# Kernel tuning notes

Hardware: AMD Instinct MI355X
Metric: run time of the kernel (lower is better)

## Reference

```python
import jax, jax.numpy as jnp
import numpy as np

Q_MAX = 127.0  # int8 symmetric range for activations


def setup_inputs() -> dict:
    key = jax.random.key(0)
    k1, k2, k3, k4 = jax.random.split(key, 4)
    B, S, D_IN, D_OUT = 4, 2048, 4096, 4096
    x = jax.random.normal(k1, (B, S, D_IN), dtype=jnp.float32)
    # int8 weights stored as int32 in range [-127, 127]
    w_q = jax.random.randint(k2, (D_OUT, D_IN), -127, 128, dtype=jnp.int32)
    # per-output-channel weight dequant scale (small positive)
    w_scale = jax.random.uniform(k3, (D_OUT,), dtype=jnp.float32, minval=0.001, maxval=0.02)
    b = jax.random.normal(k4, (D_OUT,), dtype=jnp.float32)
    return {"x": x, "w_q": w_q, "w_scale": w_scale, "b": b}


def reference(x, w_q, w_scale, b):
    # dynamic per-token symmetric quantization of activations
    act_scale = jnp.maximum(jnp.max(jnp.abs(x), axis=-1, keepdims=True), 1e-8) / Q_MAX  # [B,S,1]
    x_q = jnp.clip(jnp.round(x / act_scale), -128.0, 127.0)  # int8-valued float
    acc = jnp.einsum("bsk,nk->bsn", x_q, w_q.astype(jnp.float32))  # [B,S,D_OUT]
    # dequantize: per-token act scale * per-channel weight scale, then bias
    y = acc * act_scale * w_scale + b
    return y
```

## Files before the change

### kernel.cpp

```cpp
#include <hip/hip_runtime.h>
#include <hip/hip_bf16.h>
#include <stdint.h>

typedef int v4i __attribute__((ext_vector_type(4)));

#define TOK 8192
#define DIN 4096
#define DOUT 4096

#define NT 32

__global__ __launch_bounds__(256) void quant_rows(const float* __restrict__ x,
                                                  int8_t* __restrict__ xq,
                                                  float* __restrict__ ascale) {
    const int row = blockIdx.x;
    const int t = threadIdx.x;
    const float* __restrict__ xr = x + (size_t)row * DIN;
    float4 v[4];
    float amax = 0.0f;
#pragma unroll
    for (int i = 0; i < 4; ++i) {
        v[i] = reinterpret_cast<const float4*>(xr)[t + 256 * i];
        amax = fmaxf(amax, fmaxf(fmaxf(fabsf(v[i].x), fabsf(v[i].y)),
                                 fmaxf(fabsf(v[i].z), fabsf(v[i].w))));
    }
#pragma unroll
    for (int off = 1; off < 64; off <<= 1)
        amax = fmaxf(amax, __shfl_xor(amax, off, 64));
    __shared__ float wmax[4];
    if ((t & 63) == 0) wmax[t >> 6] = amax;
    __syncthreads();
    amax = fmaxf(fmaxf(wmax[0], wmax[1]), fmaxf(wmax[2], wmax[3]));
    const float scale = fmaxf(amax, 1e-8f) / 127.0f;
    if (t == 0) ascale[row] = scale;
    uint32_t* __restrict__ qr = reinterpret_cast<uint32_t*>(xq + (size_t)row * DIN);
#pragma unroll
    for (int i = 0; i < 4; ++i) {
        int q0 = (int)fminf(fmaxf(rintf(v[i].x / scale), -128.0f), 127.0f);
        int q1 = (int)fminf(fmaxf(rintf(v[i].y / scale), -128.0f), 127.0f);
        int q2 = (int)fminf(fmaxf(rintf(v[i].z / scale), -128.0f), 127.0f);
        int q3 = (int)fminf(fmaxf(rintf(v[i].w / scale), -128.0f), 127.0f);
        qr[t + 256 * i] = (uint32_t)((q0 & 0xFF) | ((q1 & 0xFF) << 8) |
                                     ((q2 & 0xFF) << 16) | ((q3 & 0xFF) << 24));
    }
}

__global__ __launch_bounds__(256) void pack_w(const int* __restrict__ wq,
                                              uint32_t* __restrict__ w8) {
    const size_t i = (size_t)blockIdx.x * 256 + threadIdx.x;
    int4 a = reinterpret_cast<const int4*>(wq)[i];
    w8[i] = (uint32_t)((a.x & 0xFF) | ((a.y & 0xFF) << 8) |
                       ((a.z & 0xFF) << 16) | ((a.w & 0xFF) << 24));
}

__global__ __launch_bounds__(256, 2) void gemm_i8(const int8_t* __restrict__ A,
                                                  const int8_t* __restrict__ B,
                                                  const float* __restrict__ ascale,
                                                  const float* __restrict__ wscale,
                                                  const float* __restrict__ bias,
                                                  float* __restrict__ C) {
    __shared__ __attribute__((aligned(16))) uint8_t lds[65536];
    const int tid = threadIdx.x;
    const int bn = blockIdx.x, bm = blockIdx.y;

    const int srow = tid >> 3;
    const int sp = tid & 7;
    const size_t soff0 = (size_t)srow * DIN + (size_t)(((sp ^ (srow & 7)) * 16));
    const size_t soff1 = soff0 + (size_t)32 * DIN;
    const uint32_t dst0 = (uint32_t)tid * 16u;
    const uint32_t dst1 = dst0 + 4096u;
    const int8_t* gA = A + (size_t)bm * 128 * DIN;
    const int8_t* gB = B + (size_t)bn * 128 * DIN;

#define STAGE_HALF(gmat, rbase, bufv, h, ktc)                                            \
    do {                                                                                 \
        const int8_t* _s = (gmat) + ((size_t)(h)*64 * DIN) + ((size_t)(ktc)*128);        \
        const uint32_t _d = (rbase) + (uint32_t)(bufv)*16384u + (uint32_t)(h)*8192u;     \
        __builtin_amdgcn_global_load_lds(                                                \
            (const __attribute__((address_space(1))) void*)(_s + soff0),                 \
            (__attribute__((address_space(3))) void*)(&lds[_d + dst0]), 16, 0, 0);       \
        __builtin_amdgcn_global_load_lds(                                                \
            (const __attribute__((address_space(1))) void*)(_s + soff1),                 \
            (__attribute__((address_space(3))) void*)(&lds[_d + dst1]), 16, 0, 0);       \
    } while (0)

    const int wid = tid >> 6, l = tid & 63;
    const int wm = (wid >> 1) * 64;
    const int wn = (wid & 1) * 64;
    const int lr = l & 15, lg = l >> 4;
    const uint32_t koff0 = (uint32_t)(((lg) ^ (l & 7)) * 16);
    const uint32_t koff1 = (uint32_t)(((4 + lg) ^ (l & 7)) * 16);
    const uint32_t aRd = (uint32_t)((wm + lr) * 128);
    const uint32_t bRd = 32768u + (uint32_t)((wn + lr) * 128);
    const uint32_t a0_0 = aRd + koff0, a1_0 = aRd + koff1;
    const uint32_t a0_1 = a0_0 + 16384u, a1_1 = a1_0 + 16384u;
    const uint32_t b0_0 = bRd + koff0, b1_0 = bRd + koff1;
    const uint32_t b0_1 = b0_0 + 16384u, b1_1 = b1_0 + 16384u;

    v4i acc[4][4];
#pragma unroll
    for (int i = 0; i < 4; ++i)
#pragma unroll
        for (int j = 0; j < 4; ++j) acc[i][j] = (v4i){0, 0, 0, 0};

    v4i aT[2][2], aB[2][2], bL[2][2], bR[2][2];

#define DSR(d, b, o) asm volatile("ds_read_b128 %0, %1 offset:" o : "=v"(d) : "v"(b))

#define RD_AT(A0, A1)                                          \
    do {                                                       \
        DSR(aT[0][0], A0, "0");     DSR(aT[0][1], A1, "0");    \
        DSR(aT[1][0], A0, "2048");  DSR(aT[1][1], A1, "2048"); \
    } while (0)
#define RD_AB(A0, A1)                                          \
    do {                                                       \
        DSR(aB[0][0], A0, "4096");  DSR(aB[0][1], A1, "4096"); \
        DSR(aB[1][0], A0, "6144");  DSR(aB[1][1], A1, "6144"); \
    } while (0)
#define RD_BL(B0, B1)                                          \
    do {                                                       \
        DSR(bL[0][0], B0, "0");    DSR(bL[0][1], B1, "0");     \
        DSR(bL[1][0], B0, "2048"); DSR(bL[1][1], B1, "2048");  \
    } while (0)
#define RD_BR(B0, B1)                                          \
    do {                                                       \
        DSR(bR[0][0], B0, "4096"); DSR(bR[0][1], B1, "4096");  \
        DSR(bR[1][0], B0, "6144"); DSR(bR[1][1], B1, "6144");  \
    } while (0)

#define BAR() asm volatile("s_barrier" ::: "memory")
#define LGKM0()                                                \
    do {                                                       \
        asm volatile("s_waitcnt lgkmcnt(0)" ::: "memory");     \
        __builtin_amdgcn_sched_barrier(0);                     \
    } while (0)
#define PRIO1() __builtin_amdgcn_s_setprio(1)
#define PRIO0()                                \
    do {                                       \
        __builtin_amdgcn_sched_barrier(0);     \
        __builtin_amdgcn_s_setprio(0);         \
    } while (0)
#define VM(n) asm volatile("s_waitcnt vmcnt(" #n ")" ::: "memory")

#define MFMA_K(AF, BF, MB, NB)                                                           \
    do {                                                                                 \
        _Pragma("unroll") for (int kk = 0; kk < 2; ++kk)                                 \
        _Pragma("unroll") for (int mi = 0; mi < 2; ++mi)                                 \
        _Pragma("unroll") for (int ni = 0; ni < 2; ++ni) {                               \
            acc[(MB) + mi][(NB) + ni] = __builtin_amdgcn_mfma_i32_16x16x64_i8(           \
                AF[mi][kk], BF[ni][kk], acc[(MB) + mi][(NB) + ni], 0, 0, 0);             \
        }                                                                                \
    } while (0)

    STAGE_HALF(gA, 0u, 0, 0, 0);
    STAGE_HALF(gA, 0u, 0, 1, 0);
    STAGE_HALF(gB, 32768u, 0, 0, 0);
    STAGE_HALF(gB, 32768u, 0, 1, 0);
    STAGE_HALF(gA, 0u, 1, 0, 1);
    STAGE_HALF(gA, 0u, 1, 1, 1);
    VM(4);

    for (int t = 0; t < NT / 2; ++t) {
        const int cv = 2 * t + 1;
        const int cu2 = (2 * t + 2 < NT) ? 2 * t + 2 : NT - 1;
        const int cv2 = (2 * t + 3 < NT) ? 2 * t + 3 : NT - 1;

        BAR();
        STAGE_HALF(gB, 32768u, 1, 0, cv);
        RD_AT(a0_0, a1_0); RD_BL(b0_0, b1_0);
        LGKM0();
        PRIO1();
        RD_AB(a0_0, a1_0); RD_BR(b0_0, b1_0);
        MFMA_K(aT, bL, 0, 0);
        PRIO0();

        BAR();
        STAGE_HALF(gB, 32768u, 1, 1, cv);
        LGKM0();
        PRIO1(); MFMA_K(aT, bR, 0, 2); PRIO0();

        BAR();
        STAGE_HALF(gA, 0u, 0, 0, cu2);
        LGKM0();
        PRIO1(); MFMA_K(aB, bL, 2, 0); PRIO0();

        BAR();
        STAGE_HALF(gA, 0u, 0, 1, cu2);
        LGKM0();
        PRIO1(); MFMA_K(aB, bR, 2, 2); PRIO0();
        VM(4);

        BAR();
        STAGE_HALF(gB, 32768u, 0, 0, cu2);
        RD_AT(a0_1, a1_1); RD_BL(b0_1, b1_1);
        LGKM0();
        PRIO1();
        RD_AB(a0_1, a1_1); RD_BR(b0_1, b1_1);
        MFMA_K(aT, bL, 0, 0);
        PRIO0();

        BAR();
        STAGE_HALF(gB, 32768u, 0, 1, cu2);
        LGKM0();
        PRIO1(); MFMA_K(aT, bR, 0, 2); PRIO0();

        BAR();
        STAGE_HALF(gA, 0u, 1, 0, cv2);
        LGKM0();
        PRIO1(); MFMA_K(aB, bL, 2, 0); PRIO0();

        BAR();
        STAGE_HALF(gA, 0u, 1, 1, cv2);
        LGKM0();
        PRIO1(); MFMA_K(aB, bR, 2, 2); PRIO0();
        VM(4);
    }

    asm volatile("s_waitcnt lgkmcnt(0)" ::: "memory");
    VM(0);

    const int col0 = bn * 128 + wn + lr;
    float wsv[4], bbv[4];
#pragma unroll
    for (int ni = 0; ni < 4; ++ni) {
        wsv[ni] = wscale[col0 + ni * 16];
        bbv[ni] = bias[col0 + ni * 16];
    }
    const int rbase = bm * 128 + wm + lg * 4;
#pragma unroll
    for (int mi = 0; mi < 4; ++mi) {
#pragma unroll
        for (int r = 0; r < 4; ++r) {
            const int row = rbase + mi * 16 + r;
            const float as = ascale[row];
            float* __restrict__ crow = C + (size_t)row * DOUT;
#pragma unroll
            for (int ni = 0; ni < 4; ++ni) {
                crow[col0 + ni * 16] = (float)acc[mi][ni][r] * as * wsv[ni] + bbv[ni];
            }
        }
    }
#undef STAGE_HALF
#undef DSR
#undef RD_AT
#undef RD_AB
#undef RD_BL
#undef RD_BR
#undef BAR
#undef LGKM0
#undef PRIO1
#undef PRIO0
#undef VM
#undef MFMA_K
}

extern "C" void kernel_launch(void* const* d_in, const int* in_sizes, int n_in,
                              void* d_out, int out_size, void* d_ws, size_t ws_size,
                              hipStream_t stream) {
    const float* x = (const float*)d_in[0];
    const int* wq = (const int*)d_in[1];
    const float* wscale = (const float*)d_in[2];
    const float* bias = (const float*)d_in[3];
    float* out = (float*)d_out;

    int8_t* xq = (int8_t*)d_ws;
    int8_t* w8 = xq + (size_t)TOK * DIN;
    float* ascale = (float*)(w8 + (size_t)DOUT * DIN);

    quant_rows<<<TOK, 256, 0, stream>>>(x, xq, ascale);
    pack_w<<<(int)(((size_t)DOUT * DIN / 4) / 256), 256, 0, stream>>>(wq, (uint32_t*)w8);
    gemm_i8<<<dim3(DOUT / 128, TOK / 128), 256, 0, stream>>>(xq, w8, ascale, wscale, bias, out);
}
```

Baseline: 191.4 us.

## Halve GEMM K-tile to 64 to cut LDS and double occupancy

Shrinks the K tile of the int8 GEMM from 128 to 64 bytes. This halves LDS use to 32 KB and the fragment registers, so launch bounds can request 4 blocks per CU instead of 2. The staging swizzle, read offsets, wait counts and MFMA grouping are reworked to match. The main loop runs twice as many iterations with twice the barriers per unit of work, in exchange for more resident waves to hide latency.

```diff
diff --git a/kernel.cpp b/kernel.cpp
--- a/kernel.cpp
+++ b/kernel.cpp
@@ -8,7 +8,7 @@
 #define DIN 4096
 #define DOUT 4096
 
-#define NT 32
+#define NT 64
 
 __global__ __launch_bounds__(256) void quant_rows(const float* __restrict__ x,
                                                   int8_t* __restrict__ xq,
@@ -53,49 +53,41 @@
                        ((a.z & 0xFF) << 16) | ((a.w & 0xFF) << 24));
 }
 
-__global__ __launch_bounds__(256, 2) void gemm_i8(const int8_t* __restrict__ A,
+__global__ __launch_bounds__(256, 4) void gemm_i8(const int8_t* __restrict__ A,
                                                   const int8_t* __restrict__ B,
                                                   const float* __restrict__ ascale,
                                                   const float* __restrict__ wscale,
                                                   const float* __restrict__ bias,
                                                   float* __restrict__ C) {
-    __shared__ __attribute__((aligned(16))) uint8_t lds[65536];
+    __shared__ __attribute__((aligned(16))) uint8_t lds[32768];
     const int tid = threadIdx.x;
     const int bn = blockIdx.x, bm = blockIdx.y;
 
-    const int srow = tid >> 3;
-    const int sp = tid & 7;
-    const size_t soff0 = (size_t)srow * DIN + (size_t)(((sp ^ (srow & 7)) * 16));
-    const size_t soff1 = soff0 + (size_t)32 * DIN;
+    const int srow = tid >> 2;
+    const int sp = tid & 3;
+    const size_t soff0 = (size_t)srow * DIN + (size_t)(((sp ^ ((srow >> 1) & 3)) * 16));
     const uint32_t dst0 = (uint32_t)tid * 16u;
-    const uint32_t dst1 = dst0 + 4096u;
     const int8_t* gA = A + (size_t)bm * 128 * DIN;
     const int8_t* gB = B + (size_t)bn * 128 * DIN;
 
 #define STAGE_HALF(gmat, rbase, bufv, h, ktc)                                            \
     do {                                                                                 \
-        const int8_t* _s = (gmat) + ((size_t)(h)*64 * DIN) + ((size_t)(ktc)*128);        \
-        const uint32_t _d = (rbase) + (uint32_t)(bufv)*16384u + (uint32_t)(h)*8192u;     \
+        const int8_t* _s = (gmat) + ((size_t)(h)*64 * DIN) + ((size_t)(ktc)*64);         \
+        const uint32_t _d = (rbase) + (uint32_t)(bufv)*8192u + (uint32_t)(h)*4096u;      \
         __builtin_amdgcn_global_load_lds(                                                \
             (const __attribute__((address_space(1))) void*)(_s + soff0),                 \
             (__attribute__((address_space(3))) void*)(&lds[_d + dst0]), 16, 0, 0);       \
-        __builtin_amdgcn_global_load_lds(                                                \
-            (const __attribute__((address_space(1))) void*)(_s + soff1),                 \
-            (__attribute__((address_space(3))) void*)(&lds[_d + dst1]), 16, 0, 0);       \
     } while (0)
 
     const int wid = tid >> 6, l = tid & 63;
     const int wm = (wid >> 1) * 64;
     const int wn = (wid & 1) * 64;
     const int lr = l & 15, lg = l >> 4;
-    const uint32_t koff0 = (uint32_t)(((lg) ^ (l & 7)) * 16);
-    const uint32_t koff1 = (uint32_t)(((4 + lg) ^ (l & 7)) * 16);
-    const uint32_t aRd = (uint32_t)((wm + lr) * 128);
-    const uint32_t bRd = 32768u + (uint32_t)((wn + lr) * 128);
-    const uint32_t a0_0 = aRd + koff0, a1_0 = aRd + koff1;
-    const uint32_t a0_1 = a0_0 + 16384u, a1_1 = a1_0 + 16384u;
-    const uint32_t b0_0 = bRd + koff0, b1_0 = bRd + koff1;
-    const uint32_t b0_1 = b0_0 + 16384u, b1_1 = b1_0 + 16384u;
+    const uint32_t koff = (uint32_t)((lg ^ ((lr >> 1) & 3)) * 16);
+    const uint32_t aRd0 = (uint32_t)((wm + lr) * 64) + koff;
+    const uint32_t aRd1 = aRd0 + 8192u;
+    const uint32_t bRd0 = 16384u + (uint32_t)((wn + lr) * 64) + koff;
+    const uint32_t bRd1 = bRd0 + 8192u;
 
     v4i acc[4][4];
 #pragma unroll
@@ -103,30 +95,14 @@
 #pragma unroll
         for (int j = 0; j < 4; ++j) acc[i][j] = (v4i){0, 0, 0, 0};
 
-    v4i aT[2][2], aB[2][2], bL[2][2], bR[2][2];
+    v4i aT[2], aB[2], bL[2], bR[2];
 
 #define DSR(d, b, o) asm volatile("ds_read_b128 %0, %1 offset:" o : "=v"(d) : "v"(b))
 
-#define RD_AT(A0, A1)                                          \
-    do {                                                       \
-        DSR(aT[0][0], A0, "0");     DSR(aT[0][1], A1, "0");    \
-        DSR(aT[1][0], A0, "2048");  DSR(aT[1][1], A1, "2048"); \
-    } while (0)
-#define RD_AB(A0, A1)                                          \
-    do {                                                       \
-        DSR(aB[0][0], A0, "4096");  DSR(aB[0][1], A1, "4096"); \
-        DSR(aB[1][0], A0, "6144");  DSR(aB[1][1], A1, "6144"); \
-    } while (0)
-#define RD_BL(B0, B1)                                          \
-    do {                                                       \
-        DSR(bL[0][0], B0, "0");    DSR(bL[0][1], B1, "0");     \
-        DSR(bL[1][0], B0, "2048"); DSR(bL[1][1], B1, "2048");  \
-    } while (0)
-#define RD_BR(B0, B1)                                          \
-    do {                                                       \
-        DSR(bR[0][0], B0, "4096"); DSR(bR[0][1], B1, "4096");  \
-        DSR(bR[1][0], B0, "6144"); DSR(bR[1][1], B1, "6144");  \
-    } while (0)
+#define RD_AT(Ab) do { DSR(aT[0], Ab, "0");    DSR(aT[1], Ab, "1024"); } while (0)
+#define RD_AB(Ab) do { DSR(aB[0], Ab, "2048"); DSR(aB[1], Ab, "3072"); } while (0)
+#define RD_BL(Bb) do { DSR(bL[0], Bb, "0");    DSR(bL[1], Bb, "1024"); } while (0)
+#define RD_BR(Bb) do { DSR(bR[0], Bb, "2048"); DSR(bR[1], Bb, "3072"); } while (0)
 
 #define BAR() asm volatile("s_barrier" ::: "memory")
 #define LGKM0()                                                \
@@ -142,23 +118,22 @@
     } while (0)
 #define VM(n) asm volatile("s_waitcnt vmcnt(" #n ")" ::: "memory")
 
-#define MFMA_K(AF, BF, MB, NB)                                                           \
+#define MFMA_Q(AF, BF, MB, NB)                                                           \
     do {                                                                                 \
-        _Pragma("unroll") for (int kk = 0; kk < 2; ++kk)                                 \
         _Pragma("unroll") for (int mi = 0; mi < 2; ++mi)                                 \
         _Pragma("unroll") for (int ni = 0; ni < 2; ++ni) {                               \
             acc[(MB) + mi][(NB) + ni] = __builtin_amdgcn_mfma_i32_16x16x64_i8(           \
-                AF[mi][kk], BF[ni][kk], acc[(MB) + mi][(NB) + ni], 0, 0, 0);             \
+                AF[mi], BF[ni], acc[(MB) + mi][(NB) + ni], 0, 0, 0);                     \
         }                                                                                \
     } while (0)
 
     STAGE_HALF(gA, 0u, 0, 0, 0);
     STAGE_HALF(gA, 0u, 0, 1, 0);
-    STAGE_HALF(gB, 32768u, 0, 0, 0);
-    STAGE_HALF(gB, 32768u, 0, 1, 0);
+    STAGE_HALF(gB, 16384u, 0, 0, 0);
+    STAGE_HALF(gB, 16384u, 0, 1, 0);
     STAGE_HALF(gA, 0u, 1, 0, 1);
     STAGE_HALF(gA, 0u, 1, 1, 1);
-    VM(4);
+    VM(2);
 
     for (int t = 0; t < NT / 2; ++t) {
         const int cv = 2 * t + 1;
@@ -166,54 +141,54 @@
         const int cv2 = (2 * t + 3 < NT) ? 2 * t + 3 : NT - 1;
 
         BAR();
-        STAGE_HALF(gB, 32768u, 1, 0, cv);
-        RD_AT(a0_0, a1_0); RD_BL(b0_0, b1_0);
+        STAGE_HALF(gB, 16384u, 1, 0, cv);
+        RD_AT(aRd0); RD_BL(bRd0);
         LGKM0();
         PRIO1();
-        RD_AB(a0_0, a1_0); RD_BR(b0_0, b1_0);
-        MFMA_K(aT, bL, 0, 0);
+        RD_AB(aRd0); RD_BR(bRd0);
+        MFMA_Q(aT, bL, 0, 0);
         PRIO0();
 
         BAR();
-        STAGE_HALF(gB, 32768u, 1, 1, cv);
-        LGKM0();
-        PRIO1(); MFMA_K(aT, bR, 0, 2); PRIO0();
+        STAGE_HALF(gB, 16384u, 1, 1, cv);
+        LGKM0();
+        PRIO1(); MFMA_Q(aT, bR, 0, 2); PRIO0();
 
         BAR();
         STAGE_HALF(gA, 0u, 0, 0, cu2);
         LGKM0();
-        PRIO1(); MFMA_K(aB, bL, 2, 0); PRIO0();
+        PRIO1(); MFMA_Q(aB, bL, 2, 0); PRIO0();
 
         BAR();
         STAGE_HALF(gA, 0u, 0, 1, cu2);
         LGKM0();
-        PRIO1(); MFMA_K(aB, bR, 2, 2); PRIO0();
-        VM(4);
-
-        BAR();
-        STAGE_HALF(gB, 32768u, 0, 0, cu2);
-        RD_AT(a0_1, a1_1); RD_BL(b0_1, b1_1);
+        PRIO1(); MFMA_Q(aB, bR, 2, 2); PRIO0();
+        VM(2);
+
+        BAR();
+        STAGE_HALF(gB, 16384u, 0, 0, cu2);
+        RD_AT(aRd1); RD_BL(bRd1);
         LGKM0();
         PRIO1();
-        RD_AB(a0_1, a1_1); RD_BR(b0_1, b1_1);
-        MFMA_K(aT, bL, 0, 0);
+        RD_AB(aRd1); RD_BR(bRd1);
+        MFMA_Q(aT, bL, 0, 0);
         PRIO0();
 
         BAR();
-        STAGE_HALF(gB, 32768u, 0, 1, cu2);
-        LGKM0();
-        PRIO1(); MFMA_K(aT, bR, 0, 2); PRIO0();
+        STAGE_HALF(gB, 16384u, 0, 1, cu2);
+        LGKM0();
+        PRIO1(); MFMA_Q(aT, bR, 0, 2); PRIO0();
 
         BAR();
         STAGE_HALF(gA, 0u, 1, 0, cv2);
         LGKM0();
-        PRIO1(); MFMA_K(aB, bL, 2, 0); PRIO0();
+        PRIO1(); MFMA_Q(aB, bL, 2, 0); PRIO0();
 
         BAR();
         STAGE_HALF(gA, 0u, 1, 1, cv2);
         LGKM0();
-        PRIO1(); MFMA_K(aB, bR, 2, 2); PRIO0();
-        VM(4);
+        PRIO1(); MFMA_Q(aB, bR, 2, 2); PRIO0();
+        VM(2);
     }
 
     asm volatile("s_waitcnt lgkmcnt(0)" ::: "memory");
@@ -251,7 +226,7 @@
 #undef PRIO1
 #undef PRIO0
 #undef VM
-#undef MFMA_K
+#undef MFMA_Q
 }
 
 extern "C" void kernel_launch(void* const* d_in, const int* in_sizes, int n_in,
```

New measurement: 228.0 us. 19.1% more time.
